# Performance work log

Measured on AMD Instinct MI355X. Metric: run time of the kernel, lower is better.

Reference implementation:

```python
import jax, jax.numpy as jnp
import numpy as np

N, D, NUM_CLASSES = 8192, 512, 100

def _col_normalize(z):
    # torch.std default is unbiased (ddof=1)
    mean = z.mean(axis=0)
    std = z.std(axis=0, ddof=1)
    return (z - mean) / std

def setup_inputs() -> dict:
    key = jax.random.key(0)
    k1, k2, k3 = jax.random.split(key, 3)
    z_a = jax.random.normal(k1, (N, D), dtype=jnp.float32)
    z_b = jax.random.normal(k2, (N, D), dtype=jnp.float32)
    labels = jax.random.randint(k3, (N,), 0, NUM_CLASSES, dtype=jnp.int64)
    return {"z_a": z_a, "z_b": z_b, "labels": labels}

def reference(z_a, z_b, labels):
    d = z_a.shape[1]
    z_a_norm = _col_normalize(z_a)
    z_b_norm = _col_normalize(z_b)
    # c: [N, N] cross-correlation between samples
    c = jnp.matmul(z_a_norm, z_b_norm.T) / d
    # m[i, j] = 1 if labels[i] == labels[j] else 0 (replaces per-row loop)
    m = (labels[:, None] == labels[None, :]).astype(c.dtype)
    loss = jnp.sum((c - m) ** 2)
    return loss
```

## Files before the change

### kernel.cpp

```cpp
#include <hip/hip_runtime.h>
#include <math.h>


#define NN 8192
#define DD 512
#define NC 100
#define SPLITK 16
#define NXT 10
#define NTILE 14

#define GA_B    0u
#define GB_B    1048576u
#define RTA_B   2097152u
#define RTB_B   2359296u
#define MUA_B   2621440u
#define MUB_B   2623488u
#define RSA_B   2625536u
#define RSB_B   2627584u
#define CNT_B   2629632u
#define XTA_B   4194304u
#define XTB_B   12582912u
#define MT_B    20971520u
#define PART_B  23068672u

typedef __attribute__((ext_vector_type(8))) short short8;
typedef __attribute__((ext_vector_type(4))) float f32x4;

__constant__ int c_ti[NTILE] = {0,0,0,0,1,1,1,2,2,3, 0,1,2,3};
__constant__ int c_tj[NTILE] = {0,1,2,3,1,2,3,2,3,3, 4,4,4,4};
__constant__ float c_w[NXT]  = {1.f,2.f,2.f,2.f,1.f,2.f,2.f,1.f,2.f,1.f};

#if defined(__has_builtin)
#if __has_builtin(__builtin_amdgcn_global_load_lds)
#define HAVE_GLL 1
#endif
#endif

#ifdef HAVE_GLL
__device__ __forceinline__ void async16(const void* g, void* l) {
    __builtin_amdgcn_global_load_lds(
        (const __attribute__((address_space(1))) void*)g,
        (__attribute__((address_space(3))) void*)l, 16, 0, 0);
}
#endif

__device__ __forceinline__ short f2bf_rne(float f) {
    unsigned int u = __builtin_bit_cast(unsigned int, f);
    u += 0x7fffu + ((u >> 16) & 1u);
    return (short)(u >> 16);
}

__device__ __forceinline__ float block_reduce_sum(float v) {
    __shared__ float red[8];
    int lane = threadIdx.x & 63;
    int wave = threadIdx.x >> 6;
    #pragma unroll
    for (int off = 32; off > 0; off >>= 1) v += __shfl_down(v, off, 64);
    if (lane == 0) red[wave] = v;
    __syncthreads();
    float s = 0.f;
    if (threadIdx.x == 0) {
        int nw = (blockDim.x + 63) >> 6;
        for (int w = 0; w < nw; w++) s += red[w];
    }
    return s;
}

__global__ __launch_bounds__(256) void k_prep(const float* __restrict__ A,
                                              const float* __restrict__ B,
                                              const int* __restrict__ labels,
                                              short* __restrict__ XTa,
                                              short* __restrict__ XTb,
                                              short* __restrict__ MT,
                                              float* __restrict__ out) {
    __shared__ short LT[64][72];
    int bid = blockIdx.x;
    int t = threadIdx.x;

    if (bid >= 2048) {
        int c = bid - 2048;
        if (c == 128) { if (t == 0) out[0] = 0.f; return; }
        unsigned short one = 0x3F80;
        ushort4* dst = (ushort4*)(MT + (size_t)c * NN);
        const int4* lb4 = (const int4*)labels;
        #pragma unroll
        for (int j = 0; j < 8; j++) {
            int i4 = j * 256 + t;
            int4 lb = lb4[i4];
            ushort4 v;
            v.x = (lb.x == c) ? one : (unsigned short)0;
            v.y = (lb.y == c) ? one : (unsigned short)0;
            v.z = (lb.z == c) ? one : (unsigned short)0;
            v.w = (lb.w == c) ? one : (unsigned short)0;
            dst[i4] = v;
        }
        return;
    }

    const float* X = (bid >> 10) ? B : A;
    short* XT = (bid >> 10) ? XTb : XTa;
    int rem = bid & 1023;
    int c0 = (rem >> 7) << 6;
    int k0 = (rem & 127) << 6;

    int cc = t & 15;
    int kb = t >> 4;
    #pragma unroll
    for (int s = 0; s < 4; s++) {
        int kr = kb + s * 16;
        float4 v = *(const float4*)&X[(size_t)(k0 + kr) * DD + c0 + cc * 4];
        LT[cc * 4 + 0][kr] = f2bf_rne(v.x);
        LT[cc * 4 + 1][kr] = f2bf_rne(v.y);
        LT[cc * 4 + 2][kr] = f2bf_rne(v.z);
        LT[cc * 4 + 3][kr] = f2bf_rne(v.w);
    }
    __syncthreads();
    #pragma unroll
    for (int s = 0; s < 2; s++) {
        int idx = s * 256 + t;
        int orow = idx >> 3;
        int och = idx & 7;
        *(uint4*)&XT[(size_t)(c0 + orow) * NN + k0 + och * 8] =
            *(const uint4*)&LT[orow][och * 8];
    }
}

__global__ __launch_bounds__(256, 2) void k_gram(const short* __restrict__ XTa,
                                                 const short* __restrict__ XTb,
                                                 const short* __restrict__ MT,
                                                 float* __restrict__ part) {
    __shared__ short LA[2][128 * 64];
    __shared__ short LB[2][128 * 64];

    int b = blockIdx.x;
    int xcd = b & 7;
    int idx = b >> 3;
    int grp = (idx / NTILE) * 8 + xcd;
    int tile = idx % NTILE;
    int mat = grp >> 4;
    int chunk = grp & 15;

    const short* XT = mat ? XTb : XTa;
    int ti = c_ti[tile], tj = c_tj[tile];
    const short* PA = XT + (size_t)ti * 128 * NN;
    const short* PB = (tj < 4) ? (XT + (size_t)tj * 128 * NN) : MT;
    int k0 = chunk * (NN / SPLITK);

    int t = threadIdx.x;
    int wave = t >> 6, lane = t & 63;
    int quad = lane >> 4, l16 = lane & 15;
    int x7 = l16 & 7;
    int wrow = (wave >> 1) * 64, wcol = (wave & 1) * 64;

    int srow = lane >> 3;
    int sc = (lane & 7) ^ srow;

    auto stage = [&](int buf, int kk) {
        #pragma unroll
        for (int rr = 0; rr < 4; rr++) {
            int seg = wave * 4 + rr;
            int row = seg * 8 + srow;
            const short* ga = PA + (size_t)row * NN + k0 + kk + sc * 8;
            const short* gb = PB + (size_t)row * NN + k0 + kk + sc * 8;
#ifdef HAVE_GLL
            async16(ga, &LA[buf][seg * 512]);
            async16(gb, &LB[buf][seg * 512]);
#else
            *(uint4*)&LA[buf][seg * 512 + lane * 8] = *(const uint4*)ga;
            *(uint4*)&LB[buf][seg * 512 + lane * 8] = *(const uint4*)gb;
#endif
        }
    };

    f32x4 acc[4][4];
    #pragma unroll
    for (int i = 0; i < 4; i++)
        #pragma unroll
        for (int j = 0; j < 4; j++) acc[i][j] = (f32x4)0.f;

    const int KR = NN / SPLITK;
    int cur = 0;
    stage(0, 0);
    __syncthreads();

    for (int kk = 0; kk < KR; kk += 64) {
        if (kk + 64 < KR) stage(cur ^ 1, kk + 64);
        #pragma unroll
        for (int ks = 0; ks < 2; ks++) {
            short8 a[4], bfr[4];
            #pragma unroll
            for (int mt = 0; mt < 4; mt++)
                a[mt] = *(const short8*)&LA[cur][(wrow + mt * 16 + l16) * 64 +
                                                 (((ks * 4 + quad) ^ x7) << 3)];
            #pragma unroll
            for (int nt = 0; nt < 4; nt++)
                bfr[nt] = *(const short8*)&LB[cur][(wcol + nt * 16 + l16) * 64 +
                                                   (((ks * 4 + quad) ^ x7) << 3)];
            #pragma unroll
            for (int mt = 0; mt < 4; mt++)
                #pragma unroll
                for (int nt = 0; nt < 4; nt++)
                    acc[mt][nt] = __builtin_amdgcn_mfma_f32_16x16x32_bf16(
                        a[mt], bfr[nt], acc[mt][nt], 0, 0, 0);
        }
        __syncthreads();
        cur ^= 1;
    }

    float* pbase = part + ((size_t)(mat * NTILE + tile) * SPLITK + chunk) * 16384;
    #pragma unroll
    for (int mt = 0; mt < 4; mt++)
        #pragma unroll
        for (int nt = 0; nt < 4; nt++)
            #pragma unroll
            for (int rj = 0; rj < 4; rj++) {
                int rr2 = wrow + mt * 16 + quad * 4 + rj;
                int cc2 = wcol + nt * 16 + l16;
                pbase[rr2 * 128 + cc2] = acc[mt][nt][rj];
            }
}

__global__ void k_gsum(const float* __restrict__ part,
                       float* __restrict__ Ga, float* __restrict__ Gb,
                       float* __restrict__ RTa, float* __restrict__ RTb) {
    int bid = blockIdx.x;
    int mat = bid / (NTILE * 16);
    int rr = bid % (NTILE * 16);
    int tile = rr / 16;
    int e4 = (rr % 16) * 1024 + threadIdx.x * 4;
    const float4* p = (const float4*)(part +
        (size_t)(mat * NTILE + tile) * SPLITK * 16384 + e4);
    float4 s = make_float4(0.f, 0.f, 0.f, 0.f);
    #pragma unroll
    for (int c = 0; c < SPLITK; c++) {
        float4 v = p[(size_t)c * 4096];
        s.x += v.x; s.y += v.y; s.z += v.z; s.w += v.w;
    }
    int rw = e4 >> 7, cl = e4 & 127;
    if (tile < NXT) {
        float* G = mat ? Gb : Ga;
        *(float4*)&G[(c_ti[tile] * 128 + rw) * DD + c_tj[tile] * 128 + cl] = s;
    } else {
        float* RT = mat ? RTb : RTa;
        int col = (tile - NXT) * 128 + rw;
        RT[(size_t)(cl + 0) * DD + col] = s.x;
        RT[(size_t)(cl + 1) * DD + col] = s.y;
        RT[(size_t)(cl + 2) * DD + col] = s.z;
        RT[(size_t)(cl + 3) * DD + col] = s.w;
    }
}

__global__ void k_stats(const float* __restrict__ Ga, const float* __restrict__ Gb,
                        const float* __restrict__ RTa, const float* __restrict__ RTb,
                        const int* __restrict__ labels,
                        float* mu_a, float* mu_b, float* rs_a, float* rs_b,
                        int* counts) {
    if (blockIdx.x == 2) {
        __shared__ int h[NC];
        int t = threadIdx.x;
        if (t < NC) h[t] = 0;
        __syncthreads();
        for (int i = t; i < NN; i += blockDim.x) atomicAdd(&h[labels[i]], 1);
        __syncthreads();
        if (t < NC) counts[t] = h[t];
        return;
    }
    int mat = blockIdx.x;
    int k = threadIdx.x;
    const float* RT = mat ? RTb : RTa;
    const float* G = mat ? Gb : Ga;
    float s = 0.f;
    for (int c = 0; c < 128; c++) s += RT[c * DD + k];
    float mu = s / (float)NN;
    float sumsq = G[k * DD + k];
    float var = (sumsq - (float)NN * mu * mu) / (float)(NN - 1);
    (mat ? mu_b : mu_a)[k] = mu;
    (mat ? rs_b : rs_a)[k] = rsqrtf(var);
}

__global__ void k_term(const float* __restrict__ Ga, const float* __restrict__ Gb,
                       const float* __restrict__ RTa, const float* __restrict__ RTb,
                       const float* __restrict__ mu_a, const float* __restrict__ mu_b,
                       const float* __restrict__ rs_a, const float* __restrict__ rs_b,
                       const int* __restrict__ counts, float* out) {
    int bid = blockIdx.x;
    if (bid < 256) {
        float local = 0.f;
        for (int x = bid * 256 + threadIdx.x; x < NXT * 16384; x += 256 * 256) {
            int tile = x >> 14, e = x & 16383;
            int gi = c_ti[tile] * 128 + (e >> 7);
            int gj = c_tj[tile] * 128 + (e & 127);
            float ga = rs_a[gi] * rs_a[gj] * (Ga[gi * DD + gj] - (float)NN * mu_a[gi] * mu_a[gj]);
            float gb = rs_b[gi] * rs_b[gj] * (Gb[gi * DD + gj] - (float)NN * mu_b[gi] * mu_b[gj]);
            local += c_w[tile] * ga * gb;
        }
        float s = block_reduce_sum(local);
        if (threadIdx.x == 0) atomicAdd(out, s * (1.0f / ((float)DD * (float)DD)));
    } else {
        int c = bid - 256;
        float n = (float)counts[c];
        float local = 0.f;
        for (int k = threadIdx.x; k < DD; k += 256) {
            float ta = rs_a[k] * (RTa[c * DD + k] - n * mu_a[k]);
            float tb = rs_b[k] * (RTb[c * DD + k] - n * mu_b[k]);
            local += ta * tb;
        }
        float s = block_reduce_sum(local);
        if (threadIdx.x == 0) {
            float add = s * (-2.0f / (float)DD);
            if (c == 0) {
                float t3 = 0.f;
                for (int cc = 0; cc < NC; cc++) {
                    float nc = (float)counts[cc];
                    t3 += nc * nc;
                }
                add += t3;
            }
            atomicAdd(out, add);
        }
    }
}

extern "C" void kernel_launch(void* const* d_in, const int* in_sizes, int n_in,
                              void* d_out, int out_size, void* d_ws, size_t ws_size,
                              hipStream_t stream) {
    const float* z_a = (const float*)d_in[0];
    const float* z_b = (const float*)d_in[1];
    const int* labels = (const int*)d_in[2];
    float* out = (float*)d_out;
    char* wsb = (char*)d_ws;

    float* Ga = (float*)(wsb + GA_B);
    float* Gb = (float*)(wsb + GB_B);
    float* RTa = (float*)(wsb + RTA_B);
    float* RTb = (float*)(wsb + RTB_B);
    float* mu_a = (float*)(wsb + MUA_B);
    float* mu_b = (float*)(wsb + MUB_B);
    float* rs_a = (float*)(wsb + RSA_B);
    float* rs_b = (float*)(wsb + RSB_B);
    int* counts = (int*)(wsb + CNT_B);
    short* XTa = (short*)(wsb + XTA_B);
    short* XTb = (short*)(wsb + XTB_B);
    short* MT = (short*)(wsb + MT_B);
    float* part = (float*)(wsb + PART_B);

    hipLaunchKernelGGL(k_prep, dim3(2177), dim3(256), 0, stream,
                       z_a, z_b, labels, XTa, XTb, MT, out);
    hipLaunchKernelGGL(k_gram, dim3(2 * NTILE * SPLITK), dim3(256), 0, stream,
                       XTa, XTb, MT, part);
    hipLaunchKernelGGL(k_gsum, dim3(2 * NTILE * 16), dim3(256), 0, stream,
                       part, Ga, Gb, RTa, RTb);
    hipLaunchKernelGGL(k_stats, dim3(3), dim3(512), 0, stream,
                       Ga, Gb, RTa, RTb, labels, mu_a, mu_b, rs_a, rs_b, counts);
    hipLaunchKernelGGL(k_term, dim3(356), dim3(256), 0, stream,
                       Ga, Gb, RTa, RTb, mu_a, mu_b, rs_a, rs_b, counts, out);
}
```

Baseline: 108.4 us.

## Replace split-K partial buffer with atomic accumulation and fuse stats into term kernel

The gram kernel now atomically adds its split-K partial tiles straight into the Gram and label-sum buffers, which are zeroed by extra blocks in the prep kernel. This removes the separate partial-sum reduction kernel and its large partial-buffer round trip. Per-column means and inverse stds are recomputed in every term block from shared memory, and the label histogram moves into the prep kernel, leaving three launches instead of five. The cost is many float atomics, each output element receiving 16 contributions, which can contend and makes the summation order nondeterministic. Every term block also redoes the stats work.

Result: slower. 147.9 us (+36.5%).

```diff
diff --git a/kernel.cpp b/kernel.cpp
--- a/kernel.cpp
+++ b/kernel.cpp
@@ -11,17 +11,13 @@
 
 #define GA_B    0u
 #define GB_B    1048576u
-#define RTA_B   2097152u
-#define RTB_B   2359296u
-#define MUA_B   2621440u
-#define MUB_B   2623488u
-#define RSA_B   2625536u
-#define RSB_B   2627584u
-#define CNT_B   2629632u
+#define R2A_B   2097152u
+#define R2B_B   2359296u
+#define ZERO_END 2621440u
+#define CNT_B   2621440u
 #define XTA_B   4194304u
 #define XTB_B   12582912u
 #define MT_B    20971520u
-#define PART_B  23068672u
 
 typedef __attribute__((ext_vector_type(8))) short short8;
 typedef __attribute__((ext_vector_type(4))) float f32x4;
@@ -50,8 +46,7 @@
     return (short)(u >> 16);
 }
 
-__device__ __forceinline__ float block_reduce_sum(float v) {
-    __shared__ float red[8];
+__device__ __forceinline__ float block_reduce_sum_p(float v, float* red) {
     int lane = threadIdx.x & 63;
     int wave = threadIdx.x >> 6;
     #pragma unroll
@@ -72,14 +67,33 @@
                                               short* __restrict__ XTa,
                                               short* __restrict__ XTb,
                                               short* __restrict__ MT,
+                                              float* __restrict__ zero_span,
+                                              int* __restrict__ counts,
                                               float* __restrict__ out) {
     __shared__ short LT[64][72];
+    __shared__ int hist[NC];
     int bid = blockIdx.x;
     int t = threadIdx.x;
 
     if (bid >= 2048) {
+        if (bid >= 2256) {
+            if (t < NC) hist[t] = 0;
+            __syncthreads();
+            for (int i = t; i < NN; i += 256) atomicAdd(&hist[labels[i]], 1);
+            __syncthreads();
+            if (t < NC) counts[t] = hist[t];
+            if (t == 0) out[0] = 0.f;
+            return;
+        }
+        if (bid >= 2176) {
+            int zb = bid - 2176;
+            float4* dst = (float4*)zero_span;
+            float4 z = make_float4(0.f, 0.f, 0.f, 0.f);
+            #pragma unroll
+            for (int j = 0; j < 8; j++) dst[zb * 2048 + j * 256 + t] = z;
+            return;
+        }
         int c = bid - 2048;
-        if (c == 128) { if (t == 0) out[0] = 0.f; return; }
         unsigned short one = 0x3F80;
         ushort4* dst = (ushort4*)(MT + (size_t)c * NN);
         const int4* lb4 = (const int4*)labels;
@@ -102,7 +116,6 @@
     int rem = bid & 1023;
     int c0 = (rem >> 7) << 6;
     int k0 = (rem & 127) << 6;
-
     int cc = t & 15;
     int kb = t >> 4;
     #pragma unroll
@@ -128,7 +141,10 @@
 __global__ __launch_bounds__(256, 2) void k_gram(const short* __restrict__ XTa,
                                                  const short* __restrict__ XTb,
                                                  const short* __restrict__ MT,
-                                                 float* __restrict__ part) {
+                                                 float* __restrict__ Ga,
+                                                 float* __restrict__ Gb,
+                                                 float* __restrict__ R2a,
+                                                 float* __restrict__ R2b) {
     __shared__ short LA[2][128 * 64];
     __shared__ short LB[2][128 * 64];
 
@@ -207,106 +223,87 @@
         cur ^= 1;
     }
 
-    float* pbase = part + ((size_t)(mat * NTILE + tile) * SPLITK + chunk) * 16384;
-    #pragma unroll
-    for (int mt = 0; mt < 4; mt++)
-        #pragma unroll
-        for (int nt = 0; nt < 4; nt++)
-            #pragma unroll
-            for (int rj = 0; rj < 4; rj++) {
-                int rr2 = wrow + mt * 16 + quad * 4 + rj;
-                int cc2 = wcol + nt * 16 + l16;
-                pbase[rr2 * 128 + cc2] = acc[mt][nt][rj];
-            }
-}
-
-__global__ void k_gsum(const float* __restrict__ part,
-                       float* __restrict__ Ga, float* __restrict__ Gb,
-                       float* __restrict__ RTa, float* __restrict__ RTb) {
+    if (tile < NXT) {
+        float* G = (mat ? Gb : Ga) + ((size_t)ti * 128) * DD + tj * 128;
+        #pragma unroll
+        for (int mt = 0; mt < 4; mt++)
+            #pragma unroll
+            for (int nt = 0; nt < 4; nt++)
+                #pragma unroll
+                for (int rj = 0; rj < 4; rj++) {
+                    int rr2 = wrow + mt * 16 + quad * 4 + rj;
+                    int cc2 = wcol + nt * 16 + l16;
+                    atomicAdd(&G[(size_t)rr2 * DD + cc2], acc[mt][nt][rj]);
+                }
+    } else {
+        float* R = (mat ? R2b : R2a) + (size_t)(tile - NXT) * 128 * 128;
+        #pragma unroll
+        for (int mt = 0; mt < 4; mt++)
+            #pragma unroll
+            for (int nt = 0; nt < 4; nt++)
+                #pragma unroll
+                for (int rj = 0; rj < 4; rj++) {
+                    int rr2 = wrow + mt * 16 + quad * 4 + rj;
+                    int cc2 = wcol + nt * 16 + l16;
+                    atomicAdd(&R[(size_t)rr2 * 128 + cc2], acc[mt][nt][rj]);
+                }
+    }
+}
+
+__global__ __launch_bounds__(256) void k_term(const float* __restrict__ Ga,
+                                              const float* __restrict__ Gb,
+                                              const float* __restrict__ R2a,
+                                              const float* __restrict__ R2b,
+                                              const int* __restrict__ counts,
+                                              float* __restrict__ out) {
+    __shared__ float smua[DD], smub[DD], srsa[DD], srsb[DD];
+    __shared__ float red[8];
     int bid = blockIdx.x;
-    int mat = bid / (NTILE * 16);
-    int rr = bid % (NTILE * 16);
-    int tile = rr / 16;
-    int e4 = (rr % 16) * 1024 + threadIdx.x * 4;
-    const float4* p = (const float4*)(part +
-        (size_t)(mat * NTILE + tile) * SPLITK * 16384 + e4);
-    float4 s = make_float4(0.f, 0.f, 0.f, 0.f);
-    #pragma unroll
-    for (int c = 0; c < SPLITK; c++) {
-        float4 v = p[(size_t)c * 4096];
-        s.x += v.x; s.y += v.y; s.z += v.z; s.w += v.w;
-    }
-    int rw = e4 >> 7, cl = e4 & 127;
-    if (tile < NXT) {
-        float* G = mat ? Gb : Ga;
-        *(float4*)&G[(c_ti[tile] * 128 + rw) * DD + c_tj[tile] * 128 + cl] = s;
-    } else {
-        float* RT = mat ? RTb : RTa;
-        int col = (tile - NXT) * 128 + rw;
-        RT[(size_t)(cl + 0) * DD + col] = s.x;
-        RT[(size_t)(cl + 1) * DD + col] = s.y;
-        RT[(size_t)(cl + 2) * DD + col] = s.z;
-        RT[(size_t)(cl + 3) * DD + col] = s.w;
-    }
-}
-
-__global__ void k_stats(const float* __restrict__ Ga, const float* __restrict__ Gb,
-                        const float* __restrict__ RTa, const float* __restrict__ RTb,
-                        const int* __restrict__ labels,
-                        float* mu_a, float* mu_b, float* rs_a, float* rs_b,
-                        int* counts) {
-    if (blockIdx.x == 2) {
-        __shared__ int h[NC];
-        int t = threadIdx.x;
-        if (t < NC) h[t] = 0;
-        __syncthreads();
-        for (int i = t; i < NN; i += blockDim.x) atomicAdd(&h[labels[i]], 1);
-        __syncthreads();
-        if (t < NC) counts[t] = h[t];
-        return;
-    }
-    int mat = blockIdx.x;
-    int k = threadIdx.x;
-    const float* RT = mat ? RTb : RTa;
-    const float* G = mat ? Gb : Ga;
-    float s = 0.f;
-    for (int c = 0; c < 128; c++) s += RT[c * DD + k];
-    float mu = s / (float)NN;
-    float sumsq = G[k * DD + k];
-    float var = (sumsq - (float)NN * mu * mu) / (float)(NN - 1);
-    (mat ? mu_b : mu_a)[k] = mu;
-    (mat ? rs_b : rs_a)[k] = rsqrtf(var);
-}
-
-__global__ void k_term(const float* __restrict__ Ga, const float* __restrict__ Gb,
-                       const float* __restrict__ RTa, const float* __restrict__ RTb,
-                       const float* __restrict__ mu_a, const float* __restrict__ mu_b,
-                       const float* __restrict__ rs_a, const float* __restrict__ rs_b,
-                       const int* __restrict__ counts, float* out) {
-    int bid = blockIdx.x;
-    if (bid < 256) {
+    int t = threadIdx.x;
+
+    #pragma unroll
+    for (int half = 0; half < 2; half++) {
+        int k = half * 256 + t;
+        float sa = 0.f, sb = 0.f;
+        #pragma unroll 4
+        for (int c = 0; c < 128; c++) {
+            sa += R2a[(size_t)k * 128 + c];
+            sb += R2b[(size_t)k * 128 + c];
+        }
+        float mua = sa * (1.0f / (float)NN);
+        float mub = sb * (1.0f / (float)NN);
+        float va = (Ga[(size_t)k * DD + k] - (float)NN * mua * mua) / (float)(NN - 1);
+        float vb = (Gb[(size_t)k * DD + k] - (float)NN * mub * mub) / (float)(NN - 1);
+        smua[k] = mua; smub[k] = mub;
+        srsa[k] = rsqrtf(va); srsb[k] = rsqrtf(vb);
+    }
+    __syncthreads();
+
+    if (bid < 128) {
         float local = 0.f;
-        for (int x = bid * 256 + threadIdx.x; x < NXT * 16384; x += 256 * 256) {
+        for (int x = bid * 256 + t; x < NXT * 16384; x += 128 * 256) {
             int tile = x >> 14, e = x & 16383;
             int gi = c_ti[tile] * 128 + (e >> 7);
             int gj = c_tj[tile] * 128 + (e & 127);
-            float ga = rs_a[gi] * rs_a[gj] * (Ga[gi * DD + gj] - (float)NN * mu_a[gi] * mu_a[gj]);
-            float gb = rs_b[gi] * rs_b[gj] * (Gb[gi * DD + gj] - (float)NN * mu_b[gi] * mu_b[gj]);
+            float ga = srsa[gi] * srsa[gj] *
+                       (Ga[(size_t)gi * DD + gj] - (float)NN * smua[gi] * smua[gj]);
+            float gb = srsb[gi] * srsb[gj] *
+                       (Gb[(size_t)gi * DD + gj] - (float)NN * smub[gi] * smub[gj]);
             local += c_w[tile] * ga * gb;
         }
-        float s = block_reduce_sum(local);
-        if (threadIdx.x == 0) atomicAdd(out, s * (1.0f / ((float)DD * (float)DD)));
+        float s = block_reduce_sum_p(local, red);
+        if (t == 0) atomicAdd(out, s * (1.0f / ((float)DD * (float)DD)));
     } else {
-        int c = bid - 256;
+        int c = bid - 128;
         float n = (float)counts[c];
         float local = 0.f;
-        for (int k = threadIdx.x; k < DD; k += 256) {
-            float ta = rs_a[k] * (RTa[c * DD + k] - n * mu_a[k]);
-            float tb = rs_b[k] * (RTb[c * DD + k] - n * mu_b[k]);
+        for (int k = t; k < DD; k += 256) {
+            float ta = srsa[k] * (R2a[(size_t)k * 128 + c] - n * smua[k]);
+            float tb = srsb[k] * (R2b[(size_t)k * 128 + c] - n * smub[k]);
             local += ta * tb;
         }
-        float s = block_reduce_sum(local);
-        if (threadIdx.x == 0) {
+        float s = block_reduce_sum_p(local, red);
+        if (t == 0) {
             float add = s * (-2.0f / (float)DD);
             if (c == 0) {
                 float t3 = 0.f;
@@ -332,26 +329,18 @@
 
     float* Ga = (float*)(wsb + GA_B);
     float* Gb = (float*)(wsb + GB_B);
-    float* RTa = (float*)(wsb + RTA_B);
-    float* RTb = (float*)(wsb + RTB_B);
-    float* mu_a = (float*)(wsb + MUA_B);
-    float* mu_b = (float*)(wsb + MUB_B);
-    float* rs_a = (float*)(wsb + RSA_B);
-    float* rs_b = (float*)(wsb + RSB_B);
+    float* R2a = (float*)(wsb + R2A_B);
+    float* R2b = (float*)(wsb + R2B_B);
     int* counts = (int*)(wsb + CNT_B);
     short* XTa = (short*)(wsb + XTA_B);
     short* XTb = (short*)(wsb + XTB_B);
     short* MT = (short*)(wsb + MT_B);
-    float* part = (float*)(wsb + PART_B);
-
-    hipLaunchKernelGGL(k_prep, dim3(2177), dim3(256), 0, stream,
-                       z_a, z_b, labels, XTa, XTb, MT, out);
+
+    hipLaunchKernelGGL(k_prep, dim3(2257), dim3(256), 0, stream,
+                       z_a, z_b, labels, XTa, XTb, MT,
+                       (float*)(wsb + GA_B), counts, out);
     hipLaunchKernelGGL(k_gram, dim3(2 * NTILE * SPLITK), dim3(256), 0, stream,
-                       XTa, XTb, MT, part);
-    hipLaunchKernelGGL(k_gsum, dim3(2 * NTILE * 16), dim3(256), 0, stream,
-                       part, Ga, Gb, RTa, RTb);
-    hipLaunchKernelGGL(k_stats, dim3(3), dim3(512), 0, stream,
-                       Ga, Gb, RTa, RTb, labels, mu_a, mu_b, rs_a, rs_b, counts);
-    hipLaunchKernelGGL(k_term, dim3(356), dim3(256), 0, stream,
-                       Ga, Gb, RTa, RTb, mu_a, mu_b, rs_a, rs_b, counts, out);
-}
+                       XTa, XTb, MT, Ga, Gb, R2a, R2b);
+    hipLaunchKernelGGL(k_term, dim3(228), dim3(256), 0, stream,
+                       Ga, Gb, R2a, R2b, counts, out);
+}
```
